# Kernel optimization log

Hardware: AMD Instinct MI355X
Metric: run time of the kernel (lower is better)

## Reference

```python
import jax, jax.numpy as jnp
import numpy as np

CODEBOOK_SIZE = 1024
CODEWORD_SIZE = 256
BETA = 0.1
N_INIT = 1  # embedding ~ U(-1/n, 1/n)


def setup_inputs() -> dict:
    key = jax.random.key(0)
    kx, ke = jax.random.split(key)
    x = jax.random.normal(kx, (16, 4096, CODEWORD_SIZE), dtype=jnp.float32)
    embedding = jax.random.uniform(
        ke, (CODEBOOK_SIZE, CODEWORD_SIZE), dtype=jnp.float32,
        minval=-1.0 / N_INIT, maxval=1.0 / N_INIT)
    return {"x": x, "embedding": embedding}


def reference(x, embedding):
    dist = (jnp.sum(x * x, axis=2, keepdims=True)
            + jnp.sum(embedding * embedding, axis=1)
            - 2.0 * jnp.einsum('btd,kd->btk', x, embedding))
    indexes = jnp.argmin(dist, axis=2)              # [B,T] int
    values = jnp.take(embedding, indexes, axis=0)   # gather == one_hot @ embedding
    sg = jax.lax.stop_gradient
    loss1 = jnp.mean((sg(x) - values) ** 2)         # codebook loss
    loss2 = jnp.mean((x - sg(values)) ** 2)         # commitment loss
    loss = loss1 + BETA * loss2
    values_st = x + sg(values - x)                  # straight-through
    return values_st, indexes, loss
```

## Files before the change

kernel.cpp:

```cpp
#include <hip/hip_runtime.h>
#include <stdint.h>


#define BT    65536
#define D     256
#define KCB   1024
#define BM    256
#define BN    256
#define NT    (KCB/BN)
#define BK    32
#define NSTEP (NT * (D / BK))

typedef float    f32x4 __attribute__((ext_vector_type(4)));
typedef _Float16 f16x8 __attribute__((ext_vector_type(8)));

#define GLOAD_LDS16(g, l) \
  __builtin_amdgcn_global_load_lds((const __attribute__((address_space(1))) void*)(g), \
                                   (__attribute__((address_space(3))) void*)(l), 16, 0, 0)

__global__ __launch_bounds__(256) void split_e_kernel(const float* __restrict__ E,
                                                      _Float16* __restrict__ Eh,
                                                      _Float16* __restrict__ El,
                                                      float* __restrict__ enorm,
                                                      float* __restrict__ out_loss) {
    if (blockIdx.x == 0 && threadIdx.x == 0) *out_loss = 0.f;
    const int r = blockIdx.x * 8 + (threadIdx.x >> 5);
    const size_t i0 = (size_t)r * D + (threadIdx.x & 31) * 8;
    float4 v0 = *(const float4*)(E + i0);
    float4 v1 = *(const float4*)(E + i0 + 4);
    float v[8] = {v0.x, v0.y, v0.z, v0.w, v1.x, v1.y, v1.z, v1.w};
    f16x8 h, l;
    float s = 0.f;
    #pragma unroll
    for (int j = 0; j < 8; ++j) {
        _Float16 hh = (_Float16)v[j];
        h[j] = hh;
        l[j] = (_Float16)(v[j] - (float)hh);
        s += v[j] * v[j];
    }
    *(f16x8*)(Eh + i0) = h;
    *(f16x8*)(El + i0) = l;
    #pragma unroll
    for (int off = 1; off < 32; off <<= 1) s += __shfl_xor(s, off, 64);
    if ((threadIdx.x & 31) == 0) enorm[r] = s;
}

__global__ __launch_bounds__(512, 2) void vq_mfma_kernel(
    const float* __restrict__ X,
    const _Float16* __restrict__ Eh, const _Float16* __restrict__ El,
    const float* __restrict__ enorm, const float* __restrict__ E,
    float* __restrict__ out_vals, float* __restrict__ out_idx,
    float* __restrict__ out_loss) {
    __shared__ __align__(16) float    Asf[2][BM * BK];
    __shared__ __align__(16) _Float16 Bsh[2][BN * BK];
    __shared__ __align__(16) _Float16 Bsl[2][BN * BK];
    __shared__ float s_en[KCB];
    __shared__ float s_bd[BM];
    __shared__ int   s_bi[BM];
    __shared__ float s_red[8];

    const int tid  = threadIdx.x;
    const int w    = tid >> 6;
    const int lane = tid & 63;
    const int quad = lane >> 4;
    const int l16  = lane & 15;
    const int wm   = w >> 1;
    const int wn   = w & 1;
    const int sxa  = l16 & 7;
    const int row0 = blockIdx.x * BM;

    const int sa_row = lane >> 3;
    const int sa_off = ((lane & 7) ^ sa_row) * 4;
    const int sb_row = lane >> 2;
    const int sb_off = ((((lane & 3) - (lane >> 3)) & 3) << 3);
    const int kob = ((quad + ((l16 >> 1) & 3)) & 3) << 3;

    s_en[tid]       = enorm[tid];
    s_en[tid + 512] = enorm[tid + 512];

    auto STAGE = [&](int buf, int s) {
        const int kb   = (s & 7) * BK;
        const int col0 = (s >> 3) * BN;
        #pragma unroll
        for (int t = 0; t < 4; ++t) {
            const int chunk = w * 4 + t;
            const int gr = row0 + chunk * 8 + sa_row;
            GLOAD_LDS16(X + (size_t)gr * D + kb + sa_off, &Asf[buf][chunk * 256]);
        }
        #pragma unroll
        for (int t = 0; t < 2; ++t) {
            const int chunk = w * 2 + t;
            const int gr = col0 + chunk * 16 + sb_row;
            const size_t gb = (size_t)gr * D + kb + sb_off;
            GLOAD_LDS16(Eh + gb, &Bsh[buf][chunk * 512]);
            GLOAD_LDS16(El + gb, &Bsl[buf][chunk * 512]);
        }
    };

    float rb_d[4][4];
    int   rb_i[4][4];
    #pragma unroll
    for (int i = 0; i < 4; ++i)
        #pragma unroll
        for (int r = 0; r < 4; ++r) { rb_d[i][r] = 3.4e38f; rb_i[i][r] = 0; }
    float xs = 0.f;
    f32x4 acc[4][8];

    STAGE(0, 0);
    asm volatile("s_waitcnt lgkmcnt(0)" ::: "memory");

    #pragma unroll 2
    for (int s = 0; s < NSTEP; ++s) {
        const int cur = s & 1;
        if (s + 1 < NSTEP) {
            STAGE(cur ^ 1, s + 1);
            asm volatile("s_waitcnt vmcnt(8)" ::: "memory");
        } else {
            asm volatile("s_waitcnt vmcnt(0)" ::: "memory");
        }
        __builtin_amdgcn_s_barrier();

        if ((s & 7) == 0) {
            #pragma unroll
            for (int i = 0; i < 4; ++i)
                #pragma unroll
                for (int j = 0; j < 8; ++j) acc[i][j] = (f32x4)0.0f;
        }

        const float*    As = Asf[cur];
        const _Float16* Bh = Bsh[cur];
        const _Float16* Bl = Bsl[cur];

        f16x8 ah[4], al[4];
        #pragma unroll
        for (int i = 0; i < 4; ++i) {
            const float* rp = As + (wm * 64 + i * 16 + l16) * BK;
            const f32x4 v0 = *(const f32x4*)(rp + ((((quad << 1))     ^ sxa) << 2));
            const f32x4 v1 = *(const f32x4*)(rp + ((((quad << 1) | 1) ^ sxa) << 2));
            const float f[8] = {v0.x, v0.y, v0.z, v0.w, v1.x, v1.y, v1.z, v1.w};
            #pragma unroll
            for (int e = 0; e < 8; ++e) {
                const _Float16 hh = (_Float16)f[e];
                ah[i][e] = hh;
                al[i][e] = (_Float16)(f[e] - (float)hh);
            }
            if (wn == 0 && s < 8) {
                #pragma unroll
                for (int e = 0; e < 8; ++e) xs += f[e] * f[e];
            }
        }

        __builtin_amdgcn_s_setprio(1);
        #pragma unroll
        for (int j = 0; j < 8; ++j) {
            const int n = (wn * 128 + j * 16 + l16) * BK + kob;
            const f16x8 bh = *(const f16x8*)&Bh[n];
            const f16x8 bl = *(const f16x8*)&Bl[n];
            #pragma unroll
            for (int i = 0; i < 4; ++i) {
                acc[i][j] = __builtin_amdgcn_mfma_f32_16x16x32_f16(ah[i], bh, acc[i][j], 0, 0, 0);
                acc[i][j] = __builtin_amdgcn_mfma_f32_16x16x32_f16(al[i], bh, acc[i][j], 0, 0, 0);
                acc[i][j] = __builtin_amdgcn_mfma_f32_16x16x32_f16(ah[i], bl, acc[i][j], 0, 0, 0);
            }
        }
        __builtin_amdgcn_s_setprio(0);

        if ((s & 7) == 7) {
            const int nt = s >> 3;
            #pragma unroll
            for (int j = 0; j < 8; ++j) {
                const int c = nt * BN + wn * 128 + j * 16 + l16;
                const float en = s_en[c];
                #pragma unroll
                for (int i = 0; i < 4; ++i)
                    #pragma unroll
                    for (int r = 0; r < 4; ++r) {
                        const float sd = en - 2.0f * acc[i][j][r];
                        if (sd < rb_d[i][r]) { rb_d[i][r] = sd; rb_i[i][r] = c; }
                    }
            }
        }
        __builtin_amdgcn_s_barrier();
    }

    #pragma unroll
    for (int off = 1; off < 16; off <<= 1) {
        #pragma unroll
        for (int i = 0; i < 4; ++i)
            #pragma unroll
            for (int r = 0; r < 4; ++r) {
                const float od = __shfl_xor(rb_d[i][r], off, 64);
                const int   oi = __shfl_xor(rb_i[i][r], off, 64);
                if (od < rb_d[i][r] || (od == rb_d[i][r] && oi < rb_i[i][r])) {
                    rb_d[i][r] = od; rb_i[i][r] = oi;
                }
            }
    }
    if (wn == 0 && l16 == 0) {
        #pragma unroll
        for (int i = 0; i < 4; ++i)
            #pragma unroll
            for (int r = 0; r < 4; ++r) {
                const int m = wm * 64 + i * 16 + quad * 4 + r;
                s_bd[m] = rb_d[i][r]; s_bi[m] = rb_i[i][r];
            }
    }
    __syncthreads();
    if (wn == 1 && l16 == 0) {
        #pragma unroll
        for (int i = 0; i < 4; ++i)
            #pragma unroll
            for (int r = 0; r < 4; ++r) {
                const int m = wm * 64 + i * 16 + quad * 4 + r;
                if (rb_d[i][r] < s_bd[m] || (rb_d[i][r] == s_bd[m] && rb_i[i][r] < s_bi[m])) {
                    s_bd[m] = rb_d[i][r]; s_bi[m] = rb_i[i][r];
                }
            }
    }
    __syncthreads();

    float part = xs;
    if (tid < BM) {
        out_idx[row0 + tid] = (float)s_bi[tid];
        part += s_bd[tid];
    }

    const int col = tid & 255;
    const int sub = tid >> 8;
    #pragma unroll 4
    for (int it = 0; it < BM / 2; ++it) {
        const int r  = it * 2 + sub;
        const int bi = s_bi[r];
        out_vals[(size_t)(row0 + r) * D + col] = E[(size_t)bi * D + col];
    }

    #pragma unroll
    for (int off = 1; off < 64; off <<= 1) part += __shfl_xor(part, off, 64);
    if (lane == 0) s_red[w] = part;
    __syncthreads();
    if (tid == 0) {
        float tot = 0.f;
        #pragma unroll
        for (int i = 0; i < 8; ++i) tot += s_red[i];
        atomicAdd(out_loss, tot * (1.1f / 16777216.f));
    }
}

extern "C" void kernel_launch(void* const* d_in, const int* in_sizes, int n_in,
                              void* d_out, int out_size, void* d_ws, size_t ws_size,
                              hipStream_t stream) {
    const float* X = (const float*)d_in[0];
    const float* E = (const float*)d_in[1];
    float* out      = (float*)d_out;
    float* out_vals = out;
    float* out_idx  = out + (size_t)BT * D;
    float* out_loss = out + (size_t)BT * D + BT;

    char* ws = (char*)d_ws;
    _Float16* Eh    = (_Float16*)ws;
    _Float16* El    = Eh + (size_t)KCB * D;
    float*    enorm = (float*)(El + (size_t)KCB * D);
    (void)ws_size; (void)n_in; (void)in_sizes; (void)out_size;

    split_e_kernel<<<KCB / 8, 256, 0, stream>>>(E, Eh, El, enorm, out_loss);
    vq_mfma_kernel<<<BT / BM, 512, 0, stream>>>(X, Eh, El, enorm, E,
                                                out_vals, out_idx, out_loss);
}
```

Measured before the change: 211.3 us.

## Keep split X fragments in registers and stream only codebook tiles

The X tile is loaded once through a 64-row LDS staging buffer and converted to hi/lo fp16 fragments held in registers for the whole kernel. The main loop then streams only codebook tiles (BN reduced to 128), with each warp owning 32 rows across all codewords. This removes the repeated per-step reload and hi/lo split of X and the cross-warp argmin merge. In exchange it holds more long-lived registers per thread (pah/pal), which raises spill and occupancy risk, and adds a serialized prologue for the X conversion.

Measured after the change: 193.8 us. 8.3% less time.

```diff
diff --git a/kernel.cpp b/kernel.cpp
--- a/kernel.cpp
+++ b/kernel.cpp
@@ -6,10 +6,9 @@
 #define D     256
 #define KCB   1024
 #define BM    256
-#define BN    256
-#define NT    (KCB/BN)
+#define BN    128
+#define NTT   (KCB/BN)
 #define BK    32
-#define NSTEP (NT * (D / BK))
 
 typedef float    f32x4 __attribute__((ext_vector_type(4)));
 typedef _Float16 f16x8 __attribute__((ext_vector_type(8)));
@@ -51,7 +50,7 @@
     const float* __restrict__ enorm, const float* __restrict__ E,
     float* __restrict__ out_vals, float* __restrict__ out_idx,
     float* __restrict__ out_loss) {
-    __shared__ __align__(16) float    Asf[2][BM * BK];
+    __shared__ __align__(16) float    Xs[64 * D];
     __shared__ __align__(16) _Float16 Bsh[2][BN * BK];
     __shared__ __align__(16) _Float16 Bsl[2][BN * BK];
     __shared__ float s_en[KCB];
@@ -64,129 +63,131 @@
     const int lane = tid & 63;
     const int quad = lane >> 4;
     const int l16  = lane & 15;
-    const int wm   = w >> 1;
-    const int wn   = w & 1;
     const int sxa  = l16 & 7;
     const int row0 = blockIdx.x * BM;
 
-    const int sa_row = lane >> 3;
-    const int sa_off = ((lane & 7) ^ sa_row) * 4;
     const int sb_row = lane >> 2;
     const int sb_off = ((((lane & 3) - (lane >> 3)) & 3) << 3);
     const int kob = ((quad + ((l16 >> 1) & 3)) & 3) << 3;
 
+    auto STAGE_B = [&](int buf, int col0, int kb) {
+        const int gr = col0 + w * 16 + sb_row;
+        const size_t gb = (size_t)gr * D + kb + sb_off;
+        GLOAD_LDS16(Eh + gb, &Bsh[buf][w * 512]);
+        GLOAD_LDS16(El + gb, &Bsl[buf][w * 512]);
+    };
+
     s_en[tid]       = enorm[tid];
     s_en[tid + 512] = enorm[tid + 512];
 
-    auto STAGE = [&](int buf, int s) {
-        const int kb   = (s & 7) * BK;
-        const int col0 = (s >> 3) * BN;
-        #pragma unroll
-        for (int t = 0; t < 4; ++t) {
-            const int chunk = w * 4 + t;
-            const int gr = row0 + chunk * 8 + sa_row;
-            GLOAD_LDS16(X + (size_t)gr * D + kb + sa_off, &Asf[buf][chunk * 256]);
+    STAGE_B(0, 0, 0);
+
+    f16x8 pah[2][8], pal[2][8];
+    float xs = 0.f;
+    for (int p = 0; p < 4; ++p) {
+        #pragma unroll
+        for (int rr = 0; rr < 8; ++rr) {
+            const int sr = w * 8 + rr;
+            const int gr = row0 + p * 64 + sr;
+            GLOAD_LDS16(X + (size_t)gr * D + ((lane ^ rr) << 2), &Xs[sr * D]);
         }
-        #pragma unroll
-        for (int t = 0; t < 2; ++t) {
-            const int chunk = w * 2 + t;
-            const int gr = col0 + chunk * 16 + sb_row;
-            const size_t gb = (size_t)gr * D + kb + sb_off;
-            GLOAD_LDS16(Eh + gb, &Bsh[buf][chunk * 512]);
-            GLOAD_LDS16(El + gb, &Bsl[buf][chunk * 512]);
-        }
-    };
-
-    float rb_d[4][4];
-    int   rb_i[4][4];
-    #pragma unroll
-    for (int i = 0; i < 4; ++i)
-        #pragma unroll
-        for (int r = 0; r < 4; ++r) { rb_d[i][r] = 3.4e38f; rb_i[i][r] = 0; }
-    float xs = 0.f;
-    f32x4 acc[4][8];
-
-    STAGE(0, 0);
-    asm volatile("s_waitcnt lgkmcnt(0)" ::: "memory");
-
-    #pragma unroll 2
-    for (int s = 0; s < NSTEP; ++s) {
-        const int cur = s & 1;
-        if (s + 1 < NSTEP) {
-            STAGE(cur ^ 1, s + 1);
-            asm volatile("s_waitcnt vmcnt(8)" ::: "memory");
-        } else {
-            asm volatile("s_waitcnt vmcnt(0)" ::: "memory");
+        asm volatile("s_waitcnt vmcnt(0) lgkmcnt(0)" ::: "memory");
+        __builtin_amdgcn_s_barrier();
+        if ((w >> 1) == p) {
+            const int srb = (w & 1) * 32;
+            #pragma unroll
+            for (int i = 0; i < 2; ++i) {
+                const float* rp = &Xs[(srb + i * 16 + l16) * D];
+                #pragma unroll
+                for (int kc = 0; kc < 8; ++kc) {
+                    const int c0 = kc * 8 + quad * 2;
+                    const f32x4 v0 = *(const f32x4*)(rp + (((c0)     ^ sxa) << 2));
+                    const f32x4 v1 = *(const f32x4*)(rp + (((c0 | 1) ^ sxa) << 2));
+                    const float f[8] = {v0.x, v0.y, v0.z, v0.w, v1.x, v1.y, v1.z, v1.w};
+                    #pragma unroll
+                    for (int e = 0; e < 8; ++e) {
+                        const _Float16 hh = (_Float16)f[e];
+                        pah[i][kc][e] = hh;
+                        pal[i][kc][e] = (_Float16)(f[e] - (float)hh);
+                        xs += f[e] * f[e];
+                    }
+                }
+            }
         }
         __builtin_amdgcn_s_barrier();
-
-        if ((s & 7) == 0) {
-            #pragma unroll
-            for (int i = 0; i < 4; ++i)
-                #pragma unroll
-                for (int j = 0; j < 8; ++j) acc[i][j] = (f32x4)0.0f;
+    }
+
+    float rb_d[2][4];
+    int   rb_i[2][4];
+    #pragma unroll
+    for (int i = 0; i < 2; ++i)
+        #pragma unroll
+        for (int r = 0; r < 4; ++r) { rb_d[i][r] = 3.4e38f; rb_i[i][r] = 0; }
+    f32x4 acc[2][8];
+
+    for (int nt = 0; nt < NTT; ++nt) {
+        const int col0 = nt * BN;
+        #pragma unroll
+        for (int kc = 0; kc < 8; ++kc) {
+            const int cur = kc & 1;
+            if (kc < 7) {
+                STAGE_B(cur ^ 1, col0, (kc + 1) * BK);
+                asm volatile("s_waitcnt vmcnt(2)" ::: "memory");
+            } else if (nt < NTT - 1) {
+                STAGE_B(cur ^ 1, col0 + BN, 0);
+                asm volatile("s_waitcnt vmcnt(2)" ::: "memory");
+            } else {
+                asm volatile("s_waitcnt vmcnt(0)" ::: "memory");
+            }
+            __builtin_amdgcn_s_barrier();
+
+            if (kc == 0) {
+                #pragma unroll
+                for (int i = 0; i < 2; ++i)
+                    #pragma unroll
+                    for (int j = 0; j < 8; ++j) acc[i][j] = (f32x4)0.0f;
+            }
+
+            const _Float16* Bh = Bsh[cur];
+            const _Float16* Bl = Bsl[cur];
+
+            __builtin_amdgcn_s_setprio(1);
+            #pragma unroll
+            for (int j = 0; j < 8; ++j) {
+                const int n = (j * 16 + l16) * BK + kob;
+                const f16x8 bh = *(const f16x8*)&Bh[n];
+                const f16x8 bl = *(const f16x8*)&Bl[n];
+                #pragma unroll
+                for (int i = 0; i < 2; ++i) {
+                    acc[i][j] = __builtin_amdgcn_mfma_f32_16x16x32_f16(pah[i][kc], bh, acc[i][j], 0, 0, 0);
+                    acc[i][j] = __builtin_amdgcn_mfma_f32_16x16x32_f16(pal[i][kc], bh, acc[i][j], 0, 0, 0);
+                    acc[i][j] = __builtin_amdgcn_mfma_f32_16x16x32_f16(pah[i][kc], bl, acc[i][j], 0, 0, 0);
+                }
+            }
+            __builtin_amdgcn_s_setprio(0);
+
+            if (kc == 7) {
+                #pragma unroll
+                for (int j = 0; j < 8; ++j) {
+                    const int c = col0 + j * 16 + l16;
+                    const float en = s_en[c];
+                    #pragma unroll
+                    for (int i = 0; i < 2; ++i)
+                        #pragma unroll
+                        for (int r = 0; r < 4; ++r) {
+                            const float sd = en - 2.0f * acc[i][j][r];
+                            if (sd < rb_d[i][r]) { rb_d[i][r] = sd; rb_i[i][r] = c; }
+                        }
+                }
+            }
+            __builtin_amdgcn_s_barrier();
         }
-
-        const float*    As = Asf[cur];
-        const _Float16* Bh = Bsh[cur];
-        const _Float16* Bl = Bsl[cur];
-
-        f16x8 ah[4], al[4];
-        #pragma unroll
-        for (int i = 0; i < 4; ++i) {
-            const float* rp = As + (wm * 64 + i * 16 + l16) * BK;
-            const f32x4 v0 = *(const f32x4*)(rp + ((((quad << 1))     ^ sxa) << 2));
-            const f32x4 v1 = *(const f32x4*)(rp + ((((quad << 1) | 1) ^ sxa) << 2));
-            const float f[8] = {v0.x, v0.y, v0.z, v0.w, v1.x, v1.y, v1.z, v1.w};
-            #pragma unroll
-            for (int e = 0; e < 8; ++e) {
-                const _Float16 hh = (_Float16)f[e];
-                ah[i][e] = hh;
-                al[i][e] = (_Float16)(f[e] - (float)hh);
-            }
-            if (wn == 0 && s < 8) {
-                #pragma unroll
-                for (int e = 0; e < 8; ++e) xs += f[e] * f[e];
-            }
-        }
-
-        __builtin_amdgcn_s_setprio(1);
-        #pragma unroll
-        for (int j = 0; j < 8; ++j) {
-            const int n = (wn * 128 + j * 16 + l16) * BK + kob;
-            const f16x8 bh = *(const f16x8*)&Bh[n];
-            const f16x8 bl = *(const f16x8*)&Bl[n];
-            #pragma unroll
-            for (int i = 0; i < 4; ++i) {
-                acc[i][j] = __builtin_amdgcn_mfma_f32_16x16x32_f16(ah[i], bh, acc[i][j], 0, 0, 0);
-                acc[i][j] = __builtin_amdgcn_mfma_f32_16x16x32_f16(al[i], bh, acc[i][j], 0, 0, 0);
-                acc[i][j] = __builtin_amdgcn_mfma_f32_16x16x32_f16(ah[i], bl, acc[i][j], 0, 0, 0);
-            }
-        }
-        __builtin_amdgcn_s_setprio(0);
-
-        if ((s & 7) == 7) {
-            const int nt = s >> 3;
-            #pragma unroll
-            for (int j = 0; j < 8; ++j) {
-                const int c = nt * BN + wn * 128 + j * 16 + l16;
-                const float en = s_en[c];
-                #pragma unroll
-                for (int i = 0; i < 4; ++i)
-                    #pragma unroll
-                    for (int r = 0; r < 4; ++r) {
-                        const float sd = en - 2.0f * acc[i][j][r];
-                        if (sd < rb_d[i][r]) { rb_d[i][r] = sd; rb_i[i][r] = c; }
-                    }
-            }
-        }
-        __builtin_amdgcn_s_barrier();
     }
 
     #pragma unroll
     for (int off = 1; off < 16; off <<= 1) {
         #pragma unroll
-        for (int i = 0; i < 4; ++i)
+        for (int i = 0; i < 2; ++i)
             #pragma unroll
             for (int r = 0; r < 4; ++r) {
                 const float od = __shfl_xor(rb_d[i][r], off, 64);
@@ -196,25 +197,13 @@
                 }
             }
     }
-    if (wn == 0 && l16 == 0) {
-        #pragma unroll
-        for (int i = 0; i < 4; ++i)
+    if (l16 == 0) {
+        #pragma unroll
+        for (int i = 0; i < 2; ++i)
             #pragma unroll
             for (int r = 0; r < 4; ++r) {
-                const int m = wm * 64 + i * 16 + quad * 4 + r;
+                const int m = w * 32 + i * 16 + quad * 4 + r;
                 s_bd[m] = rb_d[i][r]; s_bi[m] = rb_i[i][r];
-            }
-    }
-    __syncthreads();
-    if (wn == 1 && l16 == 0) {
-        #pragma unroll
-        for (int i = 0; i < 4; ++i)
-            #pragma unroll
-            for (int r = 0; r < 4; ++r) {
-                const int m = wm * 64 + i * 16 + quad * 4 + r;
-                if (rb_d[i][r] < s_bd[m] || (rb_d[i][r] == s_bd[m] && rb_i[i][r] < s_bi[m])) {
-                    s_bd[m] = rb_d[i][r]; s_bi[m] = rb_i[i][r];
-                }
             }
     }
     __syncthreads();
```
